# Performance work log

Measured on AMD Instinct MI355X. Metric: run time of the kernel, lower is better.

The kernel has to match this reference:

```python
import jax, jax.numpy as jnp
import numpy as np

N = 100000
E = 1600000
EPS = 1e-5


def _layer_norm(x, g, b):
    mu = jnp.mean(x, axis=-1, keepdims=True)
    var = jnp.mean((x - mu) ** 2, axis=-1, keepdims=True)
    return (x - mu) * jax.lax.rsqrt(var + EPS) * g + b


def _sage(x, src, dst, wl, bl, wr):
    # mean aggregation of neighbor messages x[src] into dst, then linear
    msg_sum = jax.ops.segment_sum(x[src], dst, num_segments=N)          # [N, d_in]
    cnt = jax.ops.segment_sum(jnp.ones((src.shape[0],), x.dtype), dst, num_segments=N)
    mean = msg_sum / jnp.maximum(cnt, 1.0)[:, None]
    return mean @ wl.T + bl + x @ wr.T  # lin_l(mean) + lin_r(x), bias only on lin_l


def setup_inputs() -> dict:
    key = jax.random.key(0)
    ks = jax.random.split(key, 16)
    dims = [(9, 64), (64, 128), (128, 128), (128, 128)]
    inp = {
        "x": jax.random.normal(ks[0], (N, 9), dtype=jnp.float32),
        "edge_index": jax.random.randint(ks[1], (2, E), 0, N, dtype=jnp.int32),
    }
    for i, (din, dout) in enumerate(dims, start=1):
        s = 1.0 / np.sqrt(din)
        inp[f"w{i}l"] = jax.random.uniform(ks[2 + 3 * i], (dout, din), jnp.float32, -s, s)
        inp[f"b{i}"] = jnp.zeros((dout,), jnp.float32)
        inp[f"w{i}r"] = jax.random.uniform(ks[3 + 3 * i], (dout, din), jnp.float32, -s, s)
        inp[f"g{i}"] = jnp.ones((dout,), jnp.float32)
        inp[f"be{i}"] = jnp.zeros((dout,), jnp.float32)
    return inp


def reference(x, edge_index,
              w1l, b1, w1r, g1, be1,
              w2l, b2, w2r, g2, be2,
              w3l, b3, w3r, g3, be3,
              w4l, b4, w4r, g4, be4):
    src, dst = edge_index[0], edge_index[1]
    h = jax.nn.relu(_layer_norm(_sage(x, src, dst, w1l, b1, w1r), g1, be1))
    h = jax.nn.relu(_layer_norm(_sage(h, src, dst, w2l, b2, w2r), g2, be2))
    h = jax.nn.relu(_layer_norm(_sage(h, src, dst, w3l, b3, w3r), g3, be3))
    h = _layer_norm(_sage(h, src, dst, w4l, b4, w4r), g4, be4)
    return h
```

## Files before the change

kernel.cpp:

```cpp
#include <hip/hip_runtime.h>
#include <hip/hip_bf16.h>
#include <math.h>

#define N_NODES 100000
#define EPS 1e-5f
#define B2SH 11
#define NPB2 2048
#define NBUCK2 ((N_NODES + NPB2 - 1) / NPB2)
#define NPART 256

typedef __attribute__((ext_vector_type(8))) short bf16x8;
typedef __attribute__((ext_vector_type(4))) float f32x4;

__device__ __forceinline__ float bflo(unsigned int u) { return __uint_as_float(u << 16); }
__device__ __forceinline__ unsigned short fbits(float f) {
    __hip_bfloat16 h = __float2bfloat16(f);
    return *reinterpret_cast<unsigned short*>(&h);
}
__device__ __forceinline__ void stv(float* p, float y) { *p = y; }
__device__ __forceinline__ void stv(__hip_bfloat16* p, float y) { *p = __float2bfloat16(y); }
__device__ __forceinline__ unsigned char f8enc(float y) {
    return (unsigned char)((unsigned int)__builtin_amdgcn_cvt_pk_fp8_f32(y, y, 0, false) & 0xffu);
}

__global__ void part_hist(const int* __restrict__ dst, int E, int* __restrict__ blkhist) {
    __shared__ int h[NBUCK2];
    int b = blockIdx.x;
    int slice = (E + NPART - 1) / NPART;
    int s0 = b * slice;
    int s1 = min(E, s0 + slice);
    for (int i = threadIdx.x; i < NBUCK2; i += 256) h[i] = 0;
    __syncthreads();
    for (int e = s0 + threadIdx.x; e < s1; e += 256) atomicAdd(&h[dst[e] >> B2SH], 1);
    __syncthreads();
    for (int i = threadIdx.x; i < NBUCK2; i += 256) blkhist[i * NPART + b] = h[i];
}

__global__ void part_offsets(const int* __restrict__ blkhist, int* __restrict__ blkoffs,
                             int* __restrict__ bbase2, int* __restrict__ row_ptr, int E) {
    __shared__ int tot[NBUCK2];
    __shared__ int sbase[NBUCK2 + 1];
    int j = threadIdx.x;
    if (j < NBUCK2) {
        int run = 0;
#pragma unroll 8
        for (int b = 0; b < NPART; ++b) {
            blkoffs[j * NPART + b] = run;
            run += blkhist[j * NPART + b];
        }
        tot[j] = run;
    }
    __syncthreads();
    if (j == 0) {
        int run = 0;
        for (int i = 0; i < NBUCK2; ++i) {
            sbase[i] = run;
            run += tot[i];
        }
        sbase[NBUCK2] = run;
        row_ptr[N_NODES] = E;
    }
    __syncthreads();
    if (j <= NBUCK2) bbase2[j] = sbase[j];
    if (j < NBUCK2) {
        int base = sbase[j];
#pragma unroll 8
        for (int b = 0; b < NPART; ++b) blkoffs[j * NPART + b] += base;
    }
}

__global__ void part_scatter(const int* __restrict__ src, const int* __restrict__ dst, int E,
                             const int* __restrict__ blkoffs, unsigned int* __restrict__ pairs) {
    __shared__ int pos[NBUCK2];
    int b = blockIdx.x;
    int slice = (E + NPART - 1) / NPART;
    int s0 = b * slice;
    int s1 = min(E, s0 + slice);
    for (int i = threadIdx.x; i < NBUCK2; i += 256) pos[i] = blkoffs[i * NPART + b];
    __syncthreads();
    for (int e = s0 + threadIdx.x; e < s1; e += 256) {
        int d = dst[e];
        int jb = d >> B2SH;
        int p = atomicAdd(&pos[jb], 1);
        pairs[p] = ((unsigned int)src[e] << B2SH) | (unsigned int)(d & (NPB2 - 1));
    }
}

__global__ __launch_bounds__(1024) void bucket_build2(const unsigned int* __restrict__ pairs,
                                                      const int* __restrict__ bbase2,
                                                      int* __restrict__ row_ptr,
                                                      int* __restrict__ col) {
    __shared__ int lcnt[NPB2];
    __shared__ int lofs[NPB2];
    __shared__ int part[1024];
    int bk = blockIdx.x;
    int base = bbase2[bk];
    int cntb = bbase2[bk + 1] - base;
    int node0 = bk << B2SH;
    int t = threadIdx.x;
    lcnt[t] = 0;
    lcnt[t + 1024] = 0;
    __syncthreads();
    for (int i = t; i < cntb; i += 1024) atomicAdd(&lcnt[pairs[base + i] & (NPB2 - 1)], 1);
    __syncthreads();
    int a0 = lcnt[2 * t], a1 = lcnt[2 * t + 1];
    part[t] = a0 + a1;
    __syncthreads();
    for (int off = 1; off < 1024; off <<= 1) {
        int v = (t >= off) ? part[t - off] : 0;
        __syncthreads();
        part[t] += v;
        __syncthreads();
    }
    int excl = part[t] - (a0 + a1);
    lofs[2 * t] = excl;
    lofs[2 * t + 1] = excl + a0;
    __syncthreads();
#pragma unroll
    for (int k = 0; k < 2; ++k) {
        int ln = 2 * t + k;
        int node = node0 + ln;
        if (node < N_NODES) row_ptr[node] = base + lofs[ln];
    }
    lcnt[t] = 0;
    lcnt[t + 1024] = 0;
    __syncthreads();
    for (int i = t; i < cntb; i += 1024) {
        unsigned int v = pairs[base + i];
        int ld = v & (NPB2 - 1);
        int s = v >> B2SH;
        int p = base + lofs[ld] + atomicAdd(&lcnt[ld], 1);
        col[p] = s;
    }
}

__global__ void agg9_kernel(const float* __restrict__ x, const int* __restrict__ row_ptr,
                            const int* __restrict__ col, float* __restrict__ mean, int n) {
    int node = (blockIdx.x * blockDim.x + threadIdx.x) >> 6;
    int lane = threadIdx.x & 63;
    int wv = threadIdx.x >> 6;
    __shared__ float red[4][64];
    float acc = 0.f;
    int start = 0, end = 0;
    if (node < n) {
        start = row_ptr[node];
        end = row_ptr[node + 1];
        int g = lane / 9;
        int f = lane - g * 9;
        if (g < 7 && end > start) {
            for (int p = start + g; p < end; p += 28) {
#pragma unroll
                for (int i = 0; i < 4; ++i) {
                    int q = p + i * 7;
                    int idx = (q < end) ? q : end - 1;
                    float v = x[(size_t)col[idx] * 9 + f];
                    if (q >= end) v = 0.f;
                    acc += v;
                }
            }
        }
    }
    red[wv][lane] = acc;
    __syncthreads();
    if (node < n && lane < 9) {
        float s = red[wv][lane];
#pragma unroll
        for (int k = 1; k < 7; ++k) s += red[wv][lane + 9 * k];
        float inv = 1.f / fmaxf((float)(end - start), 1.f);
        mean[(size_t)node * 9 + lane] = s * inv;
    }
}

__device__ __forceinline__ void acc16_fp8(const uint4& v, float* acc) {
#pragma unroll
    for (int d = 0; d < 4; ++d) {
        unsigned int u = (&v.x)[d];
        acc[d * 4 + 0] += __builtin_amdgcn_cvt_f32_fp8(u, 0);
        acc[d * 4 + 1] += __builtin_amdgcn_cvt_f32_fp8(u, 1);
        acc[d * 4 + 2] += __builtin_amdgcn_cvt_f32_fp8(u, 2);
        acc[d * 4 + 3] += __builtin_amdgcn_cvt_f32_fp8(u, 3);
    }
}

__global__ void agg64_kernel(const unsigned char* __restrict__ h8, const int* __restrict__ row_ptr,
                             const int* __restrict__ col, unsigned short* __restrict__ mean, int n) {
    int node = (blockIdx.x * blockDim.x + threadIdx.x) >> 6;
    int lane = threadIdx.x & 63;
    if (node >= n) return;
    int e = lane >> 2, c = lane & 3;
    int start = row_ptr[node], end = row_ptr[node + 1];
    int deg = end - start;
    float acc[16];
#pragma unroll
    for (int j = 0; j < 16; ++j) acc[j] = 0.f;
    const unsigned char* hc = h8 + c * 16;
    for (int p = start; p < end; p += 16) {
        int q = p + e;
        int idx = col[(q < end) ? q : end - 1];
        uint4 v = *(const uint4*)(hc + ((size_t)idx << 6));
        if (q >= end) v = (uint4){0u, 0u, 0u, 0u};
        acc16_fp8(v, acc);
    }
#pragma unroll
    for (int j = 0; j < 16; ++j) {
        acc[j] += __shfl_xor(acc[j], 4);
        acc[j] += __shfl_xor(acc[j], 8);
        acc[j] += __shfl_xor(acc[j], 16);
        acc[j] += __shfl_xor(acc[j], 32);
    }
    if (e == 0) {
        float inv = 1.f / fmaxf((float)deg, 1.f);
        unsigned int w[8];
#pragma unroll
        for (int j = 0; j < 8; ++j) {
            unsigned int lo = fbits(acc[2 * j] * inv);
            unsigned int hi = fbits(acc[2 * j + 1] * inv);
            w[j] = lo | (hi << 16);
        }
        unsigned short* mrow = mean + (size_t)node * 64 + c * 16;
        *(uint4*)(mrow) = (uint4){w[0], w[1], w[2], w[3]};
        *(uint4*)(mrow + 8) = (uint4){w[4], w[5], w[6], w[7]};
    }
}

__global__ void agg128_kernel(const unsigned char* __restrict__ h8, const int* __restrict__ row_ptr,
                              const int* __restrict__ col, unsigned short* __restrict__ mean, int n) {
    int node = (blockIdx.x * blockDim.x + threadIdx.x) >> 6;
    int lane = threadIdx.x & 63;
    if (node >= n) return;
    int e = lane >> 3, c = lane & 7;
    int start = row_ptr[node], end = row_ptr[node + 1];
    int deg = end - start;
    float acc[16];
#pragma unroll
    for (int j = 0; j < 16; ++j) acc[j] = 0.f;
    const unsigned char* hc = h8 + c * 16;
    for (int p = start; p < end; p += 16) {
        int qa = p + e;
        int qb = p + 8 + e;
        int ia = col[(qa < end) ? qa : end - 1];
        int ib = col[(qb < end) ? qb : end - 1];
        uint4 va = *(const uint4*)(hc + ((size_t)ia << 7));
        uint4 vb = *(const uint4*)(hc + ((size_t)ib << 7));
        if (qa >= end) va = (uint4){0u, 0u, 0u, 0u};
        if (qb >= end) vb = (uint4){0u, 0u, 0u, 0u};
        acc16_fp8(va, acc);
        acc16_fp8(vb, acc);
    }
#pragma unroll
    for (int j = 0; j < 16; ++j) {
        acc[j] += __shfl_xor(acc[j], 8);
        acc[j] += __shfl_xor(acc[j], 16);
        acc[j] += __shfl_xor(acc[j], 32);
    }
    if (e == 0) {
        float inv = 1.f / fmaxf((float)deg, 1.f);
        unsigned int w[8];
#pragma unroll
        for (int j = 0; j < 8; ++j) {
            unsigned int lo = fbits(acc[2 * j] * inv);
            unsigned int hi = fbits(acc[2 * j + 1] * inv);
            w[j] = lo | (hi << 16);
        }
        unsigned short* mrow = mean + (size_t)node * 128 + c * 16;
        *(uint4*)(mrow) = (uint4){w[0], w[1], w[2], w[3]};
        *(uint4*)(mrow + 8) = (uint4){w[4], w[5], w[6], w[7]};
    }
}

__global__ void wtrans_kernel(const float* __restrict__ wl, const float* __restrict__ wr,
                              int din, int dout, float* __restrict__ wt) {
    int i = blockIdx.x * blockDim.x + threadIdx.x;
    int K2 = 2 * din;
    if (i >= K2 * dout) return;
    int k = i / dout, j = i % dout;
    wt[k * dout + j] = (k < din) ? wl[j * din + k] : wr[j * din + (k - din)];
}

__global__ void packw_kernel(const float* __restrict__ wl, const float* __restrict__ wr,
                             int din, unsigned short* __restrict__ bpack) {
    int K2 = 2 * din;
    int total = K2 * 128;
    int i = blockIdx.x * 256 + threadIdx.x;
    if (i >= total) return;
    int e = i & 7;
    int lane = (i >> 3) & 63;
    int rest = i >> 9;
    int KSTEPS = din / 16;
    int t = rest / KSTEPS, ks = rest % KSTEPS;
    int j = t * 16 + (lane & 15);
    int k = ks * 32 + (lane >> 4) * 8 + e;
    float w = (k < din) ? wl[j * din + k] : wr[j * din + (k - din)];
    bpack[i] = fbits(w);
}

template <int DIN, int DOUT, bool RELU, typename OT>
__global__ __launch_bounds__(256) void linear_ln_kernel(
    const float* __restrict__ meanp, const float* __restrict__ hp,
    const float* __restrict__ wt, const float* __restrict__ bias,
    const float* __restrict__ g, const float* __restrict__ be,
    OT* __restrict__ out, unsigned char* __restrict__ out8, int n) {
    constexpr int K2 = 2 * DIN;
    constexpr int NCOL = DOUT / 4;
    constexpr int NROW = 256 / NCOL;
    constexpr int TN = 4 * NROW;
    constexpr int ASTR = TN + 4;
    constexpr int OSTR = DOUT + 4;
    constexpr int SMEMF = (K2 * ASTR > TN * OSTR) ? K2 * ASTR : TN * OSTR;
    __shared__ float smem[SMEMF];

    int tid = threadIdx.x;
    int n0base = blockIdx.x * TN;

    for (int idx = tid; idx < TN * K2; idx += 256) {
        int nn = idx / K2;
        int k = idx % K2;
        int node = n0base + nn;
        float v = 0.f;
        if (node < n)
            v = (k < DIN) ? meanp[(size_t)node * DIN + k] : hp[(size_t)node * DIN + (k - DIN)];
        smem[k * ASTR + nn] = v;
    }
    __syncthreads();

    int colt = tid % NCOL;
    int rowt = tid / NCOL;
    int j0 = colt * 4;
    int nn0 = rowt * 4;

    float acc[4][4];
#pragma unroll
    for (int i = 0; i < 4; ++i)
#pragma unroll
        for (int j = 0; j < 4; ++j) acc[i][j] = 0.f;

#pragma unroll 2
    for (int k = 0; k < K2; ++k) {
        float4 a = *(const float4*)&smem[k * ASTR + nn0];
        float4 w = *(const float4*)&wt[k * DOUT + j0];
        acc[0][0] = fmaf(a.x, w.x, acc[0][0]);
        acc[0][1] = fmaf(a.x, w.y, acc[0][1]);
        acc[0][2] = fmaf(a.x, w.z, acc[0][2]);
        acc[0][3] = fmaf(a.x, w.w, acc[0][3]);
        acc[1][0] = fmaf(a.y, w.x, acc[1][0]);
        acc[1][1] = fmaf(a.y, w.y, acc[1][1]);
        acc[1][2] = fmaf(a.y, w.z, acc[1][2]);
        acc[1][3] = fmaf(a.y, w.w, acc[1][3]);
        acc[2][0] = fmaf(a.z, w.x, acc[2][0]);
        acc[2][1] = fmaf(a.z, w.y, acc[2][1]);
        acc[2][2] = fmaf(a.z, w.z, acc[2][2]);
        acc[2][3] = fmaf(a.z, w.w, acc[2][3]);
        acc[3][0] = fmaf(a.w, w.x, acc[3][0]);
        acc[3][1] = fmaf(a.w, w.y, acc[3][1]);
        acc[3][2] = fmaf(a.w, w.z, acc[3][2]);
        acc[3][3] = fmaf(a.w, w.w, acc[3][3]);
    }
    __syncthreads();

    float4 bj = *(const float4*)&bias[j0];
#pragma unroll
    for (int i = 0; i < 4; ++i) {
        float4 o;
        o.x = acc[i][0] + bj.x;
        o.y = acc[i][1] + bj.y;
        o.z = acc[i][2] + bj.z;
        o.w = acc[i][3] + bj.w;
        *(float4*)&smem[(nn0 + i) * OSTR + j0] = o;
    }
    __syncthreads();

    int wid = tid >> 6, lane = tid & 63;
    for (int nn = wid; nn < TN; nn += 4) {
        int node = n0base + nn;
        if (node >= n) continue;
        float v0 = smem[nn * OSTR + lane];
        float v1 = (DOUT == 128) ? smem[nn * OSTR + 64 + lane] : 0.f;
        float s = v0 + v1;
        float ss = v0 * v0 + v1 * v1;
#pragma unroll
        for (int off = 32; off > 0; off >>= 1) {
            s += __shfl_xor(s, off);
            ss += __shfl_xor(ss, off);
        }
        float mu = s / DOUT;
        float var = ss / DOUT - mu * mu;
        float inv = rsqrtf(var + EPS);
        float y0 = (v0 - mu) * inv * g[lane] + be[lane];
        if (RELU) y0 = fmaxf(y0, 0.f);
        stv(&out[(size_t)node * DOUT + lane], y0);
        if (out8) out8[(size_t)node * DOUT + lane] = f8enc(y0);
        if (DOUT == 128) {
            float y1 = (v1 - mu) * inv * g[64 + lane] + be[64 + lane];
            if (RELU) y1 = fmaxf(y1, 0.f);
            stv(&out[(size_t)node * DOUT + 64 + lane], y1);
            if (out8) out8[(size_t)node * DOUT + 64 + lane] = f8enc(y1);
        }
    }
}

template <int DIN, bool RELU, typename OT>
__global__ __launch_bounds__(256) void mfma_linear_ln(
    const unsigned short* __restrict__ meanb, const unsigned short* __restrict__ hb,
    const unsigned short* __restrict__ bpack, const float* __restrict__ bias,
    const float* __restrict__ g, const float* __restrict__ be, OT* __restrict__ out,
    unsigned char* __restrict__ out8, int n) {
    constexpr int KSTEPS = DIN / 16;
    int tid = threadIdx.x;
    int w = tid >> 6, l = tid & 63;
    int n0 = blockIdx.x * 64 + w * 16;
    int arow = l & 15;
    int koff = (l >> 4) * 8;
    int anode = n0 + arow;
    if (anode >= n) anode = n - 1;
    const unsigned short* mrow = meanb + (size_t)anode * DIN;
    const unsigned short* hrow = hb + (size_t)anode * DIN;

    f32x4 acc[8];
#pragma unroll
    for (int t = 0; t < 8; ++t) acc[t] = (f32x4){0.f, 0.f, 0.f, 0.f};

#pragma unroll
    for (int ks = 0; ks < KSTEPS; ++ks) {
        int k = ks * 32 + koff;
        const unsigned short* ap = (k < DIN) ? (mrow + k) : (hrow + (k - DIN));
        bf16x8 a = *(const bf16x8*)ap;
#pragma unroll
        for (int t = 0; t < 8; ++t) {
            bf16x8 b = *(const bf16x8*)(bpack + (((size_t)t * KSTEPS + ks) * 64 + l) * 8);
            acc[t] = __builtin_amdgcn_mfma_f32_16x16x32_bf16(a, b, acc[t], 0, 0, 0);
        }
    }

    int jbase = l & 15;
    float bj[8], gj[8], bej[8];
#pragma unroll
    for (int t = 0; t < 8; ++t) {
        bj[t] = bias[t * 16 + jbase];
        gj[t] = g[t * 16 + jbase];
        bej[t] = be[t * 16 + jbase];
    }
#pragma unroll
    for (int r = 0; r < 4; ++r) {
        float v[8];
        float s = 0.f, ss = 0.f;
#pragma unroll
        for (int t = 0; t < 8; ++t) {
            v[t] = acc[t][r] + bj[t];
            s += v[t];
            ss += v[t] * v[t];
        }
#pragma unroll
        for (int off = 1; off < 16; off <<= 1) {
            s += __shfl_xor(s, off);
            ss += __shfl_xor(ss, off);
        }
        float mu = s * (1.f / 128.f);
        float var = ss * (1.f / 128.f) - mu * mu;
        float inv = rsqrtf(var + EPS);
        int node = n0 + (l >> 4) * 4 + r;
        if (node < n) {
#pragma unroll
            for (int t = 0; t < 8; ++t) {
                float y = (v[t] - mu) * inv * gj[t] + bej[t];
                if (RELU) y = fmaxf(y, 0.f);
                stv(&out[(size_t)node * 128 + t * 16 + jbase], y);
                if (out8) out8[(size_t)node * 128 + t * 16 + jbase] = f8enc(y);
            }
        }
    }
}

extern "C" void kernel_launch(void* const* d_in, const int* in_sizes, int n_in,
                              void* d_out, int out_size, void* d_ws, size_t ws_size,
                              hipStream_t stream) {
    const float* x = (const float*)d_in[0];
    const int* edge = (const int*)d_in[1];
    int E = in_sizes[1] / 2;
    const int* src = edge;
    const int* dst = edge + E;

    const float* w1l = (const float*)d_in[2];
    const float* b1  = (const float*)d_in[3];
    const float* w1r = (const float*)d_in[4];
    const float* g1  = (const float*)d_in[5];
    const float* be1 = (const float*)d_in[6];
    const float* w2l = (const float*)d_in[7];
    const float* b2  = (const float*)d_in[8];
    const float* w2r = (const float*)d_in[9];
    const float* g2  = (const float*)d_in[10];
    const float* be2 = (const float*)d_in[11];
    const float* w3l = (const float*)d_in[12];
    const float* b3  = (const float*)d_in[13];
    const float* w3r = (const float*)d_in[14];
    const float* g3  = (const float*)d_in[15];
    const float* be3 = (const float*)d_in[16];
    const float* w4l = (const float*)d_in[17];
    const float* b4  = (const float*)d_in[18];
    const float* w4r = (const float*)d_in[19];
    const float* g4  = (const float*)d_in[20];
    const float* be4 = (const float*)d_in[21];

    char* ws = (char*)d_ws;
    size_t off = 0;
    auto alloc = [&](size_t bytes) {
        void* p = ws + off;
        off = (off + bytes + 255) & ~(size_t)255;
        return p;
    };
    int* row_ptr = (int*)alloc((N_NODES + 1) * sizeof(int));
    int* blkhist = (int*)alloc((size_t)NBUCK2 * NPART * sizeof(int));
    int* blkoffs = (int*)alloc((size_t)NBUCK2 * NPART * sizeof(int));
    int* bbase2  = (int*)alloc((NBUCK2 + 1) * sizeof(int));
    unsigned int* pairs = (unsigned int*)alloc((size_t)E * sizeof(unsigned int));
    int* colx    = (int*)alloc((size_t)E * sizeof(int));
    float* wt1   = (float*)alloc(18 * 64 * sizeof(float));
    unsigned short* bp2 = (unsigned short*)alloc(128 * 128 * sizeof(short));
    unsigned short* bp3 = (unsigned short*)alloc(256 * 128 * sizeof(short));
    unsigned short* bp4 = (unsigned short*)alloc(256 * 128 * sizeof(short));
    float* m9    = (float*)alloc((size_t)N_NODES * 9 * sizeof(float));
    unsigned short* mbf = (unsigned short*)alloc((size_t)N_NODES * 128 * sizeof(short));
    unsigned short* h1  = (unsigned short*)alloc((size_t)N_NODES * 64 * sizeof(short));
    unsigned short* h2  = (unsigned short*)alloc((size_t)N_NODES * 128 * sizeof(short));
    unsigned short* h3  = (unsigned short*)alloc((size_t)N_NODES * 128 * sizeof(short));
    unsigned char* h1f8 = (unsigned char*)alloc((size_t)N_NODES * 64);
    unsigned char* h2f8 = (unsigned char*)alloc((size_t)N_NODES * 128);
    unsigned char* h3f8 = (unsigned char*)alloc((size_t)N_NODES * 128);
    (void)ws_size;

    part_hist<<<NPART, 256, 0, stream>>>(dst, E, blkhist);
    part_offsets<<<1, 64, 0, stream>>>(blkhist, blkoffs, bbase2, row_ptr, E);
    part_scatter<<<NPART, 256, 0, stream>>>(src, dst, E, blkoffs, pairs);
    bucket_build2<<<NBUCK2, 1024, 0, stream>>>(pairs, bbase2, row_ptr, colx);

    wtrans_kernel<<<(18 * 64 + 255) / 256, 256, 0, stream>>>(w1l, w1r, 9, 64, wt1);
    packw_kernel<<<(128 * 128 + 255) / 256, 256, 0, stream>>>(w2l, w2r, 64, bp2);
    packw_kernel<<<(256 * 128 + 255) / 256, 256, 0, stream>>>(w3l, w3r, 128, bp3);
    packw_kernel<<<(256 * 128 + 255) / 256, 256, 0, stream>>>(w4l, w4r, 128, bp4);

    float* out = (float*)d_out;
    int AGB = (N_NODES * 64 + 255) / 256;
    int LNB = (N_NODES + 63) / 64;

    agg9_kernel<<<AGB, 256, 0, stream>>>(x, row_ptr, colx, m9, N_NODES);
    linear_ln_kernel<9, 64, true, __hip_bfloat16><<<LNB, 256, 0, stream>>>(
        m9, x, wt1, b1, g1, be1, (__hip_bfloat16*)h1, h1f8, N_NODES);
    agg64_kernel<<<AGB, 256, 0, stream>>>(h1f8, row_ptr, colx, mbf, N_NODES);
    mfma_linear_ln<64, true, __hip_bfloat16><<<LNB, 256, 0, stream>>>(
        mbf, h1, bp2, b2, g2, be2, (__hip_bfloat16*)h2, h2f8, N_NODES);
    agg128_kernel<<<AGB, 256, 0, stream>>>(h2f8, row_ptr, colx, mbf, N_NODES);
    mfma_linear_ln<128, true, __hip_bfloat16><<<LNB, 256, 0, stream>>>(
        mbf, h2, bp3, b3, g3, be3, (__hip_bfloat16*)h3, h3f8, N_NODES);
    agg128_kernel<<<AGB, 256, 0, stream>>>(h3f8, row_ptr, colx, mbf, N_NODES);
    mfma_linear_ln<128, false, float><<<LNB, 256, 0, stream>>>(
        mbf, h3, bp4, b4, g4, be4, out, (unsigned char*)nullptr, N_NODES);
}
```

Before: 389.7 us.

## Process four nodes per wavefront in fp8 aggregation kernels with packed conversion

The 64- and 128-wide aggregation kernels now assign four destination nodes to each wavefront instead of one. Each wave issues independent gathers for all four nodes per iteration, which raises memory-level parallelism and amortizes the shuffle reduction. The fp8 unpack now uses packed two-value conversions instead of four separate single-value ones. In exchange, the loop runs to the largest degree among the four nodes, so lanes idle when degrees differ, and the four-node accumulator array raises register pressure, which may lower occupancy.

```diff
diff --git a/kernel.cpp b/kernel.cpp
--- a/kernel.cpp
+++ b/kernel.cpp
@@ -11,8 +11,8 @@
 
 typedef __attribute__((ext_vector_type(8))) short bf16x8;
 typedef __attribute__((ext_vector_type(4))) float f32x4;
-
-__device__ __forceinline__ float bflo(unsigned int u) { return __uint_as_float(u << 16); }
+typedef __attribute__((ext_vector_type(2))) float f32x2;
+
 __device__ __forceinline__ unsigned short fbits(float f) {
     __hip_bfloat16 h = __float2bfloat16(f);
     return *reinterpret_cast<unsigned short*>(&h);
@@ -175,96 +175,157 @@
 #pragma unroll
     for (int d = 0; d < 4; ++d) {
         unsigned int u = (&v.x)[d];
-        acc[d * 4 + 0] += __builtin_amdgcn_cvt_f32_fp8(u, 0);
-        acc[d * 4 + 1] += __builtin_amdgcn_cvt_f32_fp8(u, 1);
-        acc[d * 4 + 2] += __builtin_amdgcn_cvt_f32_fp8(u, 2);
-        acc[d * 4 + 3] += __builtin_amdgcn_cvt_f32_fp8(u, 3);
+        f32x2 a = __builtin_amdgcn_cvt_pk_f32_fp8(u, false);
+        f32x2 b = __builtin_amdgcn_cvt_pk_f32_fp8(u, true);
+        acc[d * 4 + 0] += a[0];
+        acc[d * 4 + 1] += a[1];
+        acc[d * 4 + 2] += b[0];
+        acc[d * 4 + 3] += b[1];
     }
 }
 
 __global__ void agg64_kernel(const unsigned char* __restrict__ h8, const int* __restrict__ row_ptr,
                              const int* __restrict__ col, unsigned short* __restrict__ mean, int n) {
-    int node = (blockIdx.x * blockDim.x + threadIdx.x) >> 6;
+    int wid = (blockIdx.x * blockDim.x + threadIdx.x) >> 6;
     int lane = threadIdx.x & 63;
-    if (node >= n) return;
     int e = lane >> 2, c = lane & 3;
-    int start = row_ptr[node], end = row_ptr[node + 1];
-    int deg = end - start;
-    float acc[16];
-#pragma unroll
-    for (int j = 0; j < 16; ++j) acc[j] = 0.f;
+    int nb = wid * 4;
+    if (nb >= n) return;
+    int s[4], en[4];
+#pragma unroll
+    for (int j = 0; j < 4; ++j) {
+        int node = nb + j;
+        if (node < n) {
+            s[j] = row_ptr[node];
+            en[j] = row_ptr[node + 1];
+        } else {
+            s[j] = 0;
+            en[j] = 0;
+        }
+    }
+    int mx = max(max(en[0] - s[0], en[1] - s[1]), max(en[2] - s[2], en[3] - s[3]));
+    float acc[4][16];
+#pragma unroll
+    for (int j = 0; j < 4; ++j)
+#pragma unroll
+        for (int k = 0; k < 16; ++k) acc[j][k] = 0.f;
     const unsigned char* hc = h8 + c * 16;
-    for (int p = start; p < end; p += 16) {
-        int q = p + e;
-        int idx = col[(q < end) ? q : end - 1];
-        uint4 v = *(const uint4*)(hc + ((size_t)idx << 6));
-        if (q >= end) v = (uint4){0u, 0u, 0u, 0u};
-        acc16_fp8(v, acc);
-    }
-#pragma unroll
-    for (int j = 0; j < 16; ++j) {
-        acc[j] += __shfl_xor(acc[j], 4);
-        acc[j] += __shfl_xor(acc[j], 8);
-        acc[j] += __shfl_xor(acc[j], 16);
-        acc[j] += __shfl_xor(acc[j], 32);
-    }
+    for (int b = 0; b < mx; b += 16) {
+        uint4 v[4];
+        bool m[4];
+#pragma unroll
+        for (int j = 0; j < 4; ++j) {
+            int q = s[j] + b + e;
+            m[j] = q < en[j];
+            int ci = m[j] ? q : s[j];
+            unsigned int cv = (unsigned int)col[ci];
+            cv = (cv < (unsigned int)n) ? cv : 0u;
+            v[j] = *(const uint4*)(hc + ((size_t)cv << 6));
+        }
+#pragma unroll
+        for (int j = 0; j < 4; ++j) {
+            if (!m[j]) v[j] = (uint4){0u, 0u, 0u, 0u};
+            acc16_fp8(v[j], acc[j]);
+        }
+    }
+#pragma unroll
+    for (int j = 0; j < 4; ++j)
+#pragma unroll
+        for (int k = 0; k < 16; ++k) {
+            acc[j][k] += __shfl_xor(acc[j][k], 4);
+            acc[j][k] += __shfl_xor(acc[j][k], 8);
+            acc[j][k] += __shfl_xor(acc[j][k], 16);
+            acc[j][k] += __shfl_xor(acc[j][k], 32);
+        }
     if (e == 0) {
-        float inv = 1.f / fmaxf((float)deg, 1.f);
-        unsigned int w[8];
-#pragma unroll
-        for (int j = 0; j < 8; ++j) {
-            unsigned int lo = fbits(acc[2 * j] * inv);
-            unsigned int hi = fbits(acc[2 * j + 1] * inv);
-            w[j] = lo | (hi << 16);
-        }
-        unsigned short* mrow = mean + (size_t)node * 64 + c * 16;
-        *(uint4*)(mrow) = (uint4){w[0], w[1], w[2], w[3]};
-        *(uint4*)(mrow + 8) = (uint4){w[4], w[5], w[6], w[7]};
+#pragma unroll
+        for (int j = 0; j < 4; ++j) {
+            int node = nb + j;
+            if (node >= n) continue;
+            float inv = 1.f / fmaxf((float)(en[j] - s[j]), 1.f);
+            unsigned int w[8];
+#pragma unroll
+            for (int k = 0; k < 8; ++k) {
+                unsigned int lo = fbits(acc[j][2 * k] * inv);
+                unsigned int hi = fbits(acc[j][2 * k + 1] * inv);
+                w[k] = lo | (hi << 16);
+            }
+            unsigned short* mrow = mean + (size_t)node * 64 + c * 16;
+            *(uint4*)(mrow) = (uint4){w[0], w[1], w[2], w[3]};
+            *(uint4*)(mrow + 8) = (uint4){w[4], w[5], w[6], w[7]};
+        }
     }
 }
 
 __global__ void agg128_kernel(const unsigned char* __restrict__ h8, const int* __restrict__ row_ptr,
                               const int* __restrict__ col, unsigned short* __restrict__ mean, int n) {
-    int node = (blockIdx.x * blockDim.x + threadIdx.x) >> 6;
+    int wid = (blockIdx.x * blockDim.x + threadIdx.x) >> 6;
     int lane = threadIdx.x & 63;
-    if (node >= n) return;
     int e = lane >> 3, c = lane & 7;
-    int start = row_ptr[node], end = row_ptr[node + 1];
-    int deg = end - start;
-    float acc[16];
-#pragma unroll
-    for (int j = 0; j < 16; ++j) acc[j] = 0.f;
+    int nb = wid * 4;
+    if (nb >= n) return;
+    int s[4], en[4];
+#pragma unroll
+    for (int j = 0; j < 4; ++j) {
+        int node = nb + j;
+        if (node < n) {
+            s[j] = row_ptr[node];
+            en[j] = row_ptr[node + 1];
+        } else {
+            s[j] = 0;
+            en[j] = 0;
+        }
+    }
+    int mx = max(max(en[0] - s[0], en[1] - s[1]), max(en[2] - s[2], en[3] - s[3]));
+    float acc[4][16];
+#pragma unroll
+    for (int j = 0; j < 4; ++j)
+#pragma unroll
+        for (int k = 0; k < 16; ++k) acc[j][k] = 0.f;
     const unsigned char* hc = h8 + c * 16;
-    for (int p = start; p < end; p += 16) {
-        int qa = p + e;
-        int qb = p + 8 + e;
-        int ia = col[(qa < end) ? qa : end - 1];
-        int ib = col[(qb < end) ? qb : end - 1];
-        uint4 va = *(const uint4*)(hc + ((size_t)ia << 7));
-        uint4 vb = *(const uint4*)(hc + ((size_t)ib << 7));
-        if (qa >= end) va = (uint4){0u, 0u, 0u, 0u};
-        if (qb >= end) vb = (uint4){0u, 0u, 0u, 0u};
-        acc16_fp8(va, acc);
-        acc16_fp8(vb, acc);
-    }
-#pragma unroll
-    for (int j = 0; j < 16; ++j) {
-        acc[j] += __shfl_xor(acc[j], 8);
-        acc[j] += __shfl_xor(acc[j], 16);
-        acc[j] += __shfl_xor(acc[j], 32);
-    }
+    for (int b = 0; b < mx; b += 8) {
+        uint4 v[4];
+        bool m[4];
+#pragma unroll
+        for (int j = 0; j < 4; ++j) {
+            int q = s[j] + b + e;
+            m[j] = q < en[j];
+            int ci = m[j] ? q : s[j];
+            unsigned int cv = (unsigned int)col[ci];
+            cv = (cv < (unsigned int)n) ? cv : 0u;
+            v[j] = *(const uint4*)(hc + ((size_t)cv << 7));
+        }
+#pragma unroll
+        for (int j = 0; j < 4; ++j) {
+            if (!m[j]) v[j] = (uint4){0u, 0u, 0u, 0u};
+            acc16_fp8(v[j], acc[j]);
+        }
+    }
+#pragma unroll
+    for (int j = 0; j < 4; ++j)
+#pragma unroll
+        for (int k = 0; k < 16; ++k) {
+            acc[j][k] += __shfl_xor(acc[j][k], 8);
+            acc[j][k] += __shfl_xor(acc[j][k], 16);
+            acc[j][k] += __shfl_xor(acc[j][k], 32);
+        }
     if (e == 0) {
-        float inv = 1.f / fmaxf((float)deg, 1.f);
-        unsigned int w[8];
-#pragma unroll
-        for (int j = 0; j < 8; ++j) {
-            unsigned int lo = fbits(acc[2 * j] * inv);
-            unsigned int hi = fbits(acc[2 * j + 1] * inv);
-            w[j] = lo | (hi << 16);
-        }
-        unsigned short* mrow = mean + (size_t)node * 128 + c * 16;
-        *(uint4*)(mrow) = (uint4){w[0], w[1], w[2], w[3]};
-        *(uint4*)(mrow + 8) = (uint4){w[4], w[5], w[6], w[7]};
+#pragma unroll
+        for (int j = 0; j < 4; ++j) {
+            int node = nb + j;
+            if (node >= n) continue;
+            float inv = 1.f / fmaxf((float)(en[j] - s[j]), 1.f);
+            unsigned int w[8];
+#pragma unroll
+            for (int k = 0; k < 8; ++k) {
+                unsigned int lo = fbits(acc[j][2 * k] * inv);
+                unsigned int hi = fbits(acc[j][2 * k + 1] * inv);
+                w[k] = lo | (hi << 16);
+            }
+            unsigned short* mrow = mean + (size_t)node * 128 + c * 16;
+            *(uint4*)(mrow) = (uint4){w[0], w[1], w[2], w[3]};
+            *(uint4*)(mrow + 8) = (uint4){w[4], w[5], w[6], w[7]};
+        }
     }
 }
 
@@ -512,7 +573,7 @@
     int* blkoffs = (int*)alloc((size_t)NBUCK2 * NPART * sizeof(int));
     int* bbase2  = (int*)alloc((NBUCK2 + 1) * sizeof(int));
     unsigned int* pairs = (unsigned int*)alloc((size_t)E * sizeof(unsigned int));
-    int* colx    = (int*)alloc((size_t)E * sizeof(int));
+    int* colx    = (int*)alloc(((size_t)E + 64) * sizeof(int));
     float* wt1   = (float*)alloc(18 * 64 * sizeof(float));
     unsigned short* bp2 = (unsigned short*)alloc(128 * 128 * sizeof(short));
     unsigned short* bp3 = (unsigned short*)alloc(256 * 128 * sizeof(short));
@@ -539,18 +600,19 @@
 
     float* out = (float*)d_out;
     int AGB = (N_NODES * 64 + 255) / 256;
+    int AGB4 = ((N_NODES + 3) / 4 * 64 + 255) / 256;
     int LNB = (N_NODES + 63) / 64;
 
     agg9_kernel<<<AGB, 256, 0, stream>>>(x, row_ptr, colx, m9, N_NODES);
     linear_ln_kernel<9, 64, true, __hip_bfloat16><<<LNB, 256, 0, stream>>>(
         m9, x, wt1, b1, g1, be1, (__hip_bfloat16*)h1, h1f8, N_NODES);
-    agg64_kernel<<<AGB, 256, 0, stream>>>(h1f8, row_ptr, colx, mbf, N_NODES);
+    agg64_kernel<<<AGB4, 256, 0, stream>>>(h1f8, row_ptr, colx, mbf, N_NODES);
     mfma_linear_ln<64, true, __hip_bfloat16><<<LNB, 256, 0, stream>>>(
         mbf, h1, bp2, b2, g2, be2, (__hip_bfloat16*)h2, h2f8, N_NODES);
-    agg128_kernel<<<AGB, 256, 0, stream>>>(h2f8, row_ptr, colx, mbf, N_NODES);
+    agg128_kernel<<<AGB4, 256, 0, stream>>>(h2f8, row_ptr, colx, mbf, N_NODES);
     mfma_linear_ln<128, true, __hip_bfloat16><<<LNB, 256, 0, stream>>>(
         mbf, h2, bp3, b3, g3, be3, (__hip_bfloat16*)h3, h3f8, N_NODES);
-    agg128_kernel<<<AGB, 256, 0, stream>>>(h3f8, row_ptr, colx, mbf, N_NODES);
+    agg128_kernel<<<AGB4, 256, 0, stream>>>(h3f8, row_ptr, colx, mbf, N_NODES);
     mfma_linear_ln<128, false, float><<<LNB, 256, 0, stream>>>(
         mbf, h3, bp4, b4, g4, be4, out, (unsigned char*)nullptr, N_NODES);
 }
```

Result: slower. 495.0 us (+27.0%).
